# Kernel optimization log

Hardware: AMD Instinct MI355X
Metric: run time of the kernel (lower is better)

The kernel has to match this reference:

```python
import jax, jax.numpy as jnp
import numpy as np

B, N, C, H = 8, 2048, 512, 8
D = C // H                      # head dim = 64
Q_LENGTHS = [1024 + 128 * i for i in range(B)]  # ragged: 1024..1920, sum below
TQ = sum(Q_LENGTHS)             # 11776 total queries


def setup_inputs() -> dict:
    key = jax.random.key(0)
    ks = jax.random.split(key, 5)
    w = 0.02  # init scale for weights
    return {
        "x": jax.random.normal(ks[0], (B, N, C), jnp.float32),
        "q": jax.random.normal(ks[1], (TQ, C), jnp.float32),
        "Wq": jax.random.normal(ks[2], (C, C), jnp.float32) * w,
        "Wkv": jax.random.normal(ks[3], (2 * C, C), jnp.float32) * w,
        "Wproj": jax.random.normal(ks[4], (C, C), jnp.float32) * w,
        "bproj": jnp.zeros((C,), jnp.float32),
        "q_lengths": jnp.array(Q_LENGTHS, jnp.int32),
        "max_q_len": max(Q_LENGTHS),
    }


def reference(x, q, Wq, Wkv, Wproj, bproj, q_lengths, max_q_len):
    # Eval path of Attention.forward: batched_sparse_attention(q, k, v, q_lengths, scale)
    # == varlen cross-attention: queries of batch b attend over all N kv tokens of batch b.
    Tq = q.shape[0]
    scale = D ** -0.5

    qh = (q @ Wq.T).reshape(Tq, H, D)                 # [Tq, H, D]
    kv = (x @ Wkv.T).reshape(B, N, 2, H, D)
    k = kv[:, :, 0]                                   # [B, N, H, D]
    v = kv[:, :, 1]                                   # [B, N, H, D]

    # ragged -> padded per-batch layout
    csum = jnp.cumsum(q_lengths)                      # [B]
    offs = jnp.concatenate([jnp.zeros((1,), csum.dtype), csum])
    tok = jnp.arange(Tq)
    q_batch = (tok[:, None] >= csum[None, :]).sum(-1)  # [Tq] batch id per query
    q_pos = tok - offs[q_batch]                        # [Tq] position within batch

    qpad = jnp.zeros((B, max_q_len, H, D), qh.dtype).at[q_batch, q_pos].set(qh)

    scores = jnp.einsum('blhd,bnhd->bhln', qpad, k) * scale  # [B, H, L, N]
    attn = jax.nn.softmax(scores, axis=-1)                   # all N keys valid
    out = jnp.einsum('bhln,bnhd->blhd', attn, v)             # [B, L, H, D]

    out = out[q_batch, q_pos].reshape(Tq, C)           # gather ragged rows back
    return out @ Wproj.T + bproj
```

## Files before the change

### kernel.cpp

```cpp
#include <hip/hip_runtime.h>
#include <hip/hip_bf16.h>
#include <math.h>

constexpr int Cc = 512;
constexpr int Hh = 8;
constexpr int Dd = 64;
constexpr int Nn = 2048;
constexpr int Bb = 8;
constexpr int GK = 512;

typedef __attribute__((ext_vector_type(8))) short short8;
typedef __attribute__((ext_vector_type(4))) float f32x4;
typedef __attribute__((ext_vector_type(16))) float f32x16;
typedef __attribute__((ext_vector_type(4))) unsigned int u32x4;
typedef __attribute__((ext_vector_type(2))) unsigned int u32x2;

#define C2SCALE 0.1803368801f

static __device__ __forceinline__ ushort f2bf(float v) {
  __hip_bfloat16 h = __float2bfloat16(v);
  return *reinterpret_cast<ushort*>(&h);
}
static __device__ __forceinline__ float bf2f(ushort u) {
  __hip_bfloat16 h = *reinterpret_cast<__hip_bfloat16*>(&u);
  return __bfloat162float(h);
}
static __device__ __forceinline__ unsigned int pk2(float f0, float f1) {
  return (unsigned int)f2bf(f0) | ((unsigned int)f2bf(f1) << 16);
}

template <int MODE, int TERMS, bool AF32, bool BF32>
__global__ __launch_bounds__(256) void mfma_nt2_kernel(
    const void* __restrict__ A0p, const void* __restrict__ A1p,
    const void* __restrict__ B0p, const void* __restrict__ B1p,
    const float* __restrict__ bias, float* __restrict__ Cf,
    ushort* __restrict__ Chi, int Nc)
{
  __shared__ ushort lAh[128 * 32];
  __shared__ ushort lBh[128 * 32];
  __shared__ ushort lAl[TERMS == 3 ? 128 * 32 : 1];
  __shared__ ushort lBl[TERMS == 3 ? 128 * 32 : 1];

  const int tid = threadIdx.x;
  const int w = tid >> 6, lane = tid & 63;
  const int c = lane & 15, g = lane >> 4;
  const int wr = (w >> 1) * 64, wc = (w & 1) * 64;
  const int m0 = blockIdx.y * 128, n0 = blockIdx.x * 128;
  const int sr = tid >> 2;
  const int sk = (tid & 3) * 8;

  short8 rAh[2], rAl[2], rBh[2], rBl[2];

  auto ldf32 = [&](const float* F, size_t idx, short8& h, short8& l) {
    const float4 f0 = *(const float4*)(F + idx);
    const float4 f1 = *(const float4*)(F + idx + 4);
    const float vv[8] = {f0.x, f0.y, f0.z, f0.w, f1.x, f1.y, f1.z, f1.w};
#pragma unroll
    for (int j = 0; j < 8; ++j) {
      const ushort hb = f2bf(vv[j]);
      ((ushort*)&h)[j] = hb;
      if (TERMS == 3) ((ushort*)&l)[j] = f2bf(vv[j] - bf2f(hb));
    }
  };

  auto loadA = [&](int k0) {
#pragma unroll
    for (int hf = 0; hf < 2; ++hf) {
      const size_t idx = (size_t)(m0 + sr + hf * 64) * GK + k0 + sk;
      if (AF32) {
        ldf32((const float*)A0p, idx, rAh[hf], rAl[hf]);
      } else {
        rAh[hf] = *(const short8*)((const ushort*)A0p + idx);
        if (TERMS == 3) rAl[hf] = *(const short8*)((const ushort*)A1p + idx);
      }
    }
  };
  auto loadB = [&](int k0) {
#pragma unroll
    for (int hf = 0; hf < 2; ++hf) {
      const size_t idx = (size_t)(n0 + sr + hf * 64) * GK + k0 + sk;
      if (BF32) {
        ldf32((const float*)B0p, idx, rBh[hf], rBl[hf]);
      } else {
        rBh[hf] = *(const short8*)((const ushort*)B0p + idx);
        if (TERMS == 3) rBl[hf] = *(const short8*)((const ushort*)B1p + idx);
      }
    }
  };

  f32x4 acc[4][4] = {};
  loadA(0);
  loadB(0);

  for (int k0 = 0; k0 < GK; k0 += 32) {
    __syncthreads();
    *(short8*)&lAh[sr * 32 + sk]        = rAh[0];
    *(short8*)&lAh[(sr + 64) * 32 + sk] = rAh[1];
    *(short8*)&lBh[sr * 32 + sk]        = rBh[0];
    *(short8*)&lBh[(sr + 64) * 32 + sk] = rBh[1];
    if (TERMS == 3) {
      *(short8*)&lAl[sr * 32 + sk]        = rAl[0];
      *(short8*)&lAl[(sr + 64) * 32 + sk] = rAl[1];
      *(short8*)&lBl[sr * 32 + sk]        = rBl[0];
      *(short8*)&lBl[(sr + 64) * 32 + sk] = rBl[1];
    }
    __syncthreads();
    if (k0 + 32 < GK) { loadA(k0 + 32); loadB(k0 + 32); }

    short8 ah[4], al[4], bh[4], bl[4];
#pragma unroll
    for (int i = 0; i < 4; ++i) {
      const int ar = (wr + i * 16 + c) * 32 + g * 8;
      const int br = (wc + i * 16 + c) * 32 + g * 8;
      ah[i] = *(const short8*)&lAh[ar];
      bh[i] = *(const short8*)&lBh[br];
      if (TERMS == 3) {
        al[i] = *(const short8*)&lAl[ar];
        bl[i] = *(const short8*)&lBl[br];
      }
    }
#pragma unroll
    for (int mi = 0; mi < 4; ++mi)
#pragma unroll
      for (int nj = 0; nj < 4; ++nj) {
        if (TERMS == 3) {
          acc[mi][nj] = __builtin_amdgcn_mfma_f32_16x16x32_bf16(ah[mi], bl[nj], acc[mi][nj], 0,0,0);
          acc[mi][nj] = __builtin_amdgcn_mfma_f32_16x16x32_bf16(al[mi], bh[nj], acc[mi][nj], 0,0,0);
        }
        acc[mi][nj] = __builtin_amdgcn_mfma_f32_16x16x32_bf16(ah[mi], bh[nj], acc[mi][nj], 0,0,0);
      }
  }

#pragma unroll
  for (int mi = 0; mi < 4; ++mi) {
#pragma unroll
    for (int r = 0; r < 4; ++r) {
      const size_t rb = (size_t)(m0 + wr + mi * 16 + g * 4 + r) * Nc;
#pragma unroll
      for (int nj = 0; nj < 4; ++nj) {
        const int col = n0 + wc + nj * 16 + c;
        const float v = acc[mi][nj][r];
        if (MODE == 0) {
          Cf[rb + col] = v + bias[col];
        } else if (MODE == 1) {
          Chi[rb + col] = f2bf(v);
        } else {
          Chi[rb + col] = f2bf(v * C2SCALE);
        }
      }
    }
  }
}


__global__ __launch_bounds__(256) void attn_mfma8_kernel(
    const ushort* __restrict__ qhi,
    const ushort* __restrict__ kbf,
    const ushort* __restrict__ vtb,
    ushort* __restrict__ ohi,
    ushort* __restrict__ olo)
{
  constexpr int QOFF[8] = {0, 1024, 2176, 3456, 4864, 6400, 8064, 9856};

  const int lin = blockIdx.x;
  const int b  = lin & 7;
  const int h  = (lin >> 3) & 7;
  const int qt = lin >> 6;

  const int Lb  = 1024 + 128 * b;
  const int off = QOFF[b];
  if (qt * 128 >= Lb) return;

  constexpr int KP = 72;
  constexpr int VP = 136;
  constexpr int NC = Nn / 128;
  __shared__ ushort Ks[128 * KP];
  __shared__ ushort Vs[64 * VP];

  const int tid = threadIdx.x;
  const int lane = tid & 63;
  const int w = tid >> 6;
  const int l31 = lane & 31;
  const int hi5 = lane >> 5;

  short8 qfh[4];
  const int qrow = off + qt * 128 + w * 32 + l31;
  {
    const size_t base = (size_t)qrow * Cc + h * Dd + hi5 * 8;
#pragma unroll
    for (int db = 0; db < 4; ++db)
      qfh[db] = *(const short8*)(qhi + base + db * 16);
  }

  float l_s = 0.f;
  f32x16 accO[2] = {};

  const size_t kbase = (size_t)b * Nn * Cc + h * Dd;
  const size_t vbase = (size_t)h * Dd * (Bb * Nn) + (size_t)b * Nn;

  for (int ch = 0; ch < NC; ++ch) {
    __syncthreads();
#pragma unroll
    for (int it = 0; it < 4; ++it) {
      const int i = tid + it * 256;
      const int row = i >> 3, c8 = (i & 7) * 8;
      *(short8*)&Ks[row * KP + c8] =
          *(const short8*)&kbf[kbase + (size_t)(ch * 128 + row) * Cc + c8];
    }
#pragma unroll
    for (int it = 0; it < 4; ++it) {
      const int i = tid + it * 256;
      const int row = i >> 4, c8 = (i & 15) * 8;
      *(short8*)&Vs[row * VP + c8] =
          *(const short8*)&vtb[vbase + (size_t)row * (Bb * Nn) + ch * 128 + c8];
    }
    __syncthreads();

#pragma unroll
    for (int st = 0; st < 2; ++st) {
      f32x16 accT[2] = {};
      __builtin_amdgcn_s_setprio(1);
#pragma unroll
      for (int db = 0; db < 4; ++db) {
#pragma unroll
        for (int kb = 0; kb < 2; ++kb) {
          const short8 kf = *(const short8*)
              &Ks[(st * 64 + kb * 32 + l31) * KP + db * 16 + hi5 * 8];
          accT[kb] = __builtin_amdgcn_mfma_f32_32x32x16_bf16(kf, qfh[db], accT[kb], 0,0,0);
        }
      }
      __builtin_amdgcn_s_setprio(0);

      float ps[4] = {0.f, 0.f, 0.f, 0.f};
#pragma unroll
      for (int kb = 0; kb < 2; ++kb)
#pragma unroll
        for (int r = 0; r < 16; ++r) {
          const float p = __builtin_amdgcn_exp2f(accT[kb][r]);
          accT[kb][r] = p;
          ps[r & 3] += p;
        }
      float psum = (ps[0] + ps[1]) + (ps[2] + ps[3]);
#if __has_builtin(__builtin_amdgcn_permlane32_swap)
      {
        const unsigned int pu = __builtin_bit_cast(unsigned int, psum);
        const u32x2 pr = __builtin_amdgcn_permlane32_swap(pu, pu, false, false);
        psum += __builtin_bit_cast(float, hi5 ? pr[0] : pr[1]);
      }
#else
      psum += __shfl_xor(psum, 32);
#endif
      l_s += psum;

      short8 pa[4];
#pragma unroll
      for (int ks = 0; ks < 4; ++ks) {
        const int kb = ks >> 1, base = (ks & 1) * 8;
        const unsigned int ua = pk2(accT[kb][base + 0], accT[kb][base + 1]);
        const unsigned int uc = pk2(accT[kb][base + 2], accT[kb][base + 3]);
        const unsigned int ub = pk2(accT[kb][base + 4], accT[kb][base + 5]);
        const unsigned int ud = pk2(accT[kb][base + 6], accT[kb][base + 7]);
        u32x4 wv;
#if __has_builtin(__builtin_amdgcn_permlane32_swap)
        const u32x2 r02 = __builtin_amdgcn_permlane32_swap(ua, ub, false, false);
        const u32x2 r13 = __builtin_amdgcn_permlane32_swap(uc, ud, false, false);
        wv.x = r02[0];
        wv.y = r13[0];
        wv.z = r02[1];
        wv.w = r13[1];
#else
        const unsigned int sxa = __shfl_xor(ua, 32);
        const unsigned int sxb = __shfl_xor(ub, 32);
        const unsigned int sxc = __shfl_xor(uc, 32);
        const unsigned int sxd = __shfl_xor(ud, 32);
        wv.x = hi5 ? sxb : ua;
        wv.y = hi5 ? sxd : uc;
        wv.z = hi5 ? ub : sxa;
        wv.w = hi5 ? ud : sxc;
#endif
        pa[ks] = __builtin_bit_cast(short8, wv);
      }

      __builtin_amdgcn_s_setprio(1);
#pragma unroll
      for (int ks = 0; ks < 4; ++ks)
#pragma unroll
        for (int ma = 0; ma < 2; ++ma) {
          const short8 vf = *(const short8*)
              &Vs[(ma * 32 + l31) * VP + st * 64 + ks * 16 + hi5 * 8];
          accO[ma] = __builtin_amdgcn_mfma_f32_32x32x16_bf16(vf, pa[ks], accO[ma], 0,0,0);
        }
      __builtin_amdgcn_s_setprio(0);
    }
  }

  const float inv = 1.f / l_s;
  const size_t rb = (size_t)qrow * Cc + h * Dd;
#pragma unroll
  for (int ma = 0; ma < 2; ++ma) {
#pragma unroll
    for (int g2 = 0; g2 < 4; ++g2) {
      const int d0 = ma * 32 + g2 * 8 + hi5 * 4;
      ushort4 uh, ul;
#pragma unroll
      for (int e = 0; e < 4; ++e) {
        const float o = accO[ma][g2 * 4 + e] * inv;
        const ushort hb = f2bf(o);
        ((ushort*)&uh)[e] = hb;
        ((ushort*)&ul)[e] = f2bf(o - bf2f(hb));
      }
      *(ushort4*)&ohi[rb + d0] = uh;
      *(ushort4*)&olo[rb + d0] = ul;
    }
  }
}

extern "C" void kernel_launch(void* const* d_in, const int* in_sizes, int n_in,
                              void* d_out, int out_size, void* d_ws, size_t ws_size,
                              hipStream_t stream)
{
  const float* x     = (const float*)d_in[0];
  const float* q     = (const float*)d_in[1];
  const float* Wq    = (const float*)d_in[2];
  const float* Wkv   = (const float*)d_in[3];
  const float* Wproj = (const float*)d_in[4];
  const float* bproj = (const float*)d_in[5];

  const int TQ = in_sizes[1] / Cc;
  const int BN = in_sizes[0] / Cc;

  const float* Wv = Wkv + (size_t)Cc * Cc;

  const size_t szQ = (size_t)TQ * Cc * 2;
  const size_t szX = (size_t)BN * Cc * 2;

  char* p = (char*)d_ws;
  ushort* q_hi  = (ushort*)p;  p += szQ;
  ushort* k_bf  = (ushort*)p;  p += szX;
  ushort* v_t   = (ushort*)p;  p += szX;
  ushort* at_hi = (ushort*)p;  p += szQ;
  ushort* at_lo = (ushort*)p;

  mfma_nt2_kernel<2, 1, true, true><<<dim3(Cc/128, TQ/128), 256, 0, stream>>>(
      q, nullptr, Wq, nullptr, nullptr, nullptr, q_hi, Cc);
  mfma_nt2_kernel<1, 1, true, true><<<dim3(Cc/128, BN/128), 256, 0, stream>>>(
      x, nullptr, Wkv, nullptr, nullptr, nullptr, k_bf, Cc);
  mfma_nt2_kernel<1, 1, true, true><<<dim3(BN/128, Cc/128), 256, 0, stream>>>(
      Wv, nullptr, x, nullptr, nullptr, nullptr, v_t, BN);
  attn_mfma8_kernel<<<dim3(64 * 15), 256, 0, stream>>>(
      q_hi, k_bf, v_t, at_hi, at_lo);
  mfma_nt2_kernel<0, 3, false, true><<<dim3(Cc/128, TQ/128), 256, 0, stream>>>(
      at_hi, at_lo, Wproj, nullptr, bproj, (float*)d_out, nullptr, Cc);
}
```

Before: 199.9 us.

## Switch attention to 16x16x32 MFMA with 512-thread blocks and permuted V layout

Rewrites the attention kernel to use 16x16x32 bf16 MFMAs with 8 waves of 16 query rows each, instead of 4 waves of 32 rows using 32x32x16. V is stored into shared memory with a column permutation, so the P accumulator registers can feed the PV MFMA directly without permlane swaps. The row sum is reduced once at the end with shuffles. The intent is to cut the cross-lane shuffle work, lower register pressure and raise occupancy, at the cost of more MFMA instructions and more waves per block.

```diff
diff --git a/kernel.cpp b/kernel.cpp
--- a/kernel.cpp
+++ b/kernel.cpp
@@ -11,7 +11,6 @@
 
 typedef __attribute__((ext_vector_type(8))) short short8;
 typedef __attribute__((ext_vector_type(4))) float f32x4;
-typedef __attribute__((ext_vector_type(16))) float f32x16;
 typedef __attribute__((ext_vector_type(4))) unsigned int u32x4;
 typedef __attribute__((ext_vector_type(2))) unsigned int u32x2;
 
@@ -152,8 +151,7 @@
   }
 }
 
-
-__global__ __launch_bounds__(256) void attn_mfma8_kernel(
+__global__ __launch_bounds__(512, 4) void attn_mfma10_kernel(
     const ushort* __restrict__ qhi,
     const ushort* __restrict__ kbf,
     const ushort* __restrict__ vtb,
@@ -180,20 +178,19 @@
   const int tid = threadIdx.x;
   const int lane = tid & 63;
   const int w = tid >> 6;
-  const int l31 = lane & 31;
-  const int hi5 = lane >> 5;
-
-  short8 qfh[4];
-  const int qrow = off + qt * 128 + w * 32 + l31;
+  const int c = lane & 15;
+  const int g = (lane >> 4) & 3;
+
+  short8 qf[2];
+  const int qrow = off + qt * 128 + w * 16 + c;
   {
-    const size_t base = (size_t)qrow * Cc + h * Dd + hi5 * 8;
-#pragma unroll
-    for (int db = 0; db < 4; ++db)
-      qfh[db] = *(const short8*)(qhi + base + db * 16);
-  }
-
-  float l_s = 0.f;
-  f32x16 accO[2] = {};
+    const size_t base = (size_t)qrow * Cc + h * Dd + g * 8;
+    qf[0] = *(const short8*)(qhi + base);
+    qf[1] = *(const short8*)(qhi + base + 32);
+  }
+
+  float l_part = 0.f;
+  f32x4 accO4[4] = {};
 
   const size_t kbase = (size_t)b * Nn * Cc + h * Dd;
   const size_t vbase = (size_t)h * Dd * (Bb * Nn) + (size_t)b * Nn;
@@ -201,117 +198,93 @@
   for (int ch = 0; ch < NC; ++ch) {
     __syncthreads();
 #pragma unroll
-    for (int it = 0; it < 4; ++it) {
-      const int i = tid + it * 256;
+    for (int it = 0; it < 2; ++it) {
+      const int i = tid + it * 512;
       const int row = i >> 3, c8 = (i & 7) * 8;
       *(short8*)&Ks[row * KP + c8] =
           *(const short8*)&kbf[kbase + (size_t)(ch * 128 + row) * Cc + c8];
     }
 #pragma unroll
-    for (int it = 0; it < 4; ++it) {
-      const int i = tid + it * 256;
+    for (int it = 0; it < 2; ++it) {
+      const int i = tid + it * 512;
       const int row = i >> 4, c8 = (i & 15) * 8;
-      *(short8*)&Vs[row * VP + c8] =
+      const short8 v =
           *(const short8*)&vtb[vbase + (size_t)row * (Bb * Nn) + ch * 128 + c8];
+      const u32x4 vv = __builtin_bit_cast(u32x4, v);
+      u32x2 vlo, vhi;
+      vlo[0] = vv[0]; vlo[1] = vv[1];
+      vhi[0] = vv[2]; vhi[1] = vv[3];
+      const int base = (c8 & ~31) | ((c8 & 8) << 1) | ((c8 & 16) >> 2);
+      *(u32x2*)&Vs[row * VP + base]     = vlo;
+      *(u32x2*)&Vs[row * VP + base + 8] = vhi;
     }
     __syncthreads();
 
 #pragma unroll
     for (int st = 0; st < 2; ++st) {
-      f32x16 accT[2] = {};
+      f32x4 accT4[4] = {};
       __builtin_amdgcn_s_setprio(1);
 #pragma unroll
-      for (int db = 0; db < 4; ++db) {
-#pragma unroll
-        for (int kb = 0; kb < 2; ++kb) {
+      for (int ks2 = 0; ks2 < 2; ++ks2) {
+#pragma unroll
+        for (int kb = 0; kb < 4; ++kb) {
           const short8 kf = *(const short8*)
-              &Ks[(st * 64 + kb * 32 + l31) * KP + db * 16 + hi5 * 8];
-          accT[kb] = __builtin_amdgcn_mfma_f32_32x32x16_bf16(kf, qfh[db], accT[kb], 0,0,0);
+              &Ks[(st * 64 + kb * 16 + c) * KP + ks2 * 32 + g * 8];
+          accT4[kb] = __builtin_amdgcn_mfma_f32_16x16x32_bf16(kf, qf[ks2], accT4[kb], 0,0,0);
         }
       }
       __builtin_amdgcn_s_setprio(0);
 
-      float ps[4] = {0.f, 0.f, 0.f, 0.f};
-#pragma unroll
-      for (int kb = 0; kb < 2; ++kb)
-#pragma unroll
-        for (int r = 0; r < 16; ++r) {
-          const float p = __builtin_amdgcn_exp2f(accT[kb][r]);
-          accT[kb][r] = p;
-          ps[r & 3] += p;
+      unsigned int up[4][2];
+#pragma unroll
+      for (int kb = 0; kb < 4; ++kb) {
+        const float p0 = __builtin_amdgcn_exp2f(accT4[kb][0]);
+        const float p1 = __builtin_amdgcn_exp2f(accT4[kb][1]);
+        const float p2 = __builtin_amdgcn_exp2f(accT4[kb][2]);
+        const float p3 = __builtin_amdgcn_exp2f(accT4[kb][3]);
+        l_part += (p0 + p1) + (p2 + p3);
+        up[kb][0] = pk2(p0, p1);
+        up[kb][1] = pk2(p2, p3);
+      }
+
+#pragma unroll
+      for (int ks2 = 0; ks2 < 2; ++ks2) {
+        u32x4 wv;
+        wv.x = up[2 * ks2][0];
+        wv.y = up[2 * ks2][1];
+        wv.z = up[2 * ks2 + 1][0];
+        wv.w = up[2 * ks2 + 1][1];
+        const short8 pa = __builtin_bit_cast(short8, wv);
+        __builtin_amdgcn_s_setprio(1);
+#pragma unroll
+        for (int db = 0; db < 4; ++db) {
+          const short8 vf = *(const short8*)
+              &Vs[(db * 16 + c) * VP + st * 64 + ks2 * 32 + g * 8];
+          accO4[db] = __builtin_amdgcn_mfma_f32_16x16x32_bf16(vf, pa, accO4[db], 0,0,0);
         }
-      float psum = (ps[0] + ps[1]) + (ps[2] + ps[3]);
-#if __has_builtin(__builtin_amdgcn_permlane32_swap)
-      {
-        const unsigned int pu = __builtin_bit_cast(unsigned int, psum);
-        const u32x2 pr = __builtin_amdgcn_permlane32_swap(pu, pu, false, false);
-        psum += __builtin_bit_cast(float, hi5 ? pr[0] : pr[1]);
-      }
-#else
-      psum += __shfl_xor(psum, 32);
-#endif
-      l_s += psum;
-
-      short8 pa[4];
-#pragma unroll
-      for (int ks = 0; ks < 4; ++ks) {
-        const int kb = ks >> 1, base = (ks & 1) * 8;
-        const unsigned int ua = pk2(accT[kb][base + 0], accT[kb][base + 1]);
-        const unsigned int uc = pk2(accT[kb][base + 2], accT[kb][base + 3]);
-        const unsigned int ub = pk2(accT[kb][base + 4], accT[kb][base + 5]);
-        const unsigned int ud = pk2(accT[kb][base + 6], accT[kb][base + 7]);
-        u32x4 wv;
-#if __has_builtin(__builtin_amdgcn_permlane32_swap)
-        const u32x2 r02 = __builtin_amdgcn_permlane32_swap(ua, ub, false, false);
-        const u32x2 r13 = __builtin_amdgcn_permlane32_swap(uc, ud, false, false);
-        wv.x = r02[0];
-        wv.y = r13[0];
-        wv.z = r02[1];
-        wv.w = r13[1];
-#else
-        const unsigned int sxa = __shfl_xor(ua, 32);
-        const unsigned int sxb = __shfl_xor(ub, 32);
-        const unsigned int sxc = __shfl_xor(uc, 32);
-        const unsigned int sxd = __shfl_xor(ud, 32);
-        wv.x = hi5 ? sxb : ua;
-        wv.y = hi5 ? sxd : uc;
-        wv.z = hi5 ? ub : sxa;
-        wv.w = hi5 ? ud : sxc;
-#endif
-        pa[ks] = __builtin_bit_cast(short8, wv);
-      }
-
-      __builtin_amdgcn_s_setprio(1);
-#pragma unroll
-      for (int ks = 0; ks < 4; ++ks)
-#pragma unroll
-        for (int ma = 0; ma < 2; ++ma) {
-          const short8 vf = *(const short8*)
-              &Vs[(ma * 32 + l31) * VP + st * 64 + ks * 16 + hi5 * 8];
-          accO[ma] = __builtin_amdgcn_mfma_f32_32x32x16_bf16(vf, pa[ks], accO[ma], 0,0,0);
-        }
-      __builtin_amdgcn_s_setprio(0);
-    }
-  }
-
-  const float inv = 1.f / l_s;
+        __builtin_amdgcn_s_setprio(0);
+      }
+    }
+  }
+
+  float l = l_part;
+  l += __shfl_xor(l, 16);
+  l += __shfl_xor(l, 32);
+  const float inv = 1.f / l;
   const size_t rb = (size_t)qrow * Cc + h * Dd;
 #pragma unroll
-  for (int ma = 0; ma < 2; ++ma) {
-#pragma unroll
-    for (int g2 = 0; g2 < 4; ++g2) {
-      const int d0 = ma * 32 + g2 * 8 + hi5 * 4;
-      ushort4 uh, ul;
-#pragma unroll
-      for (int e = 0; e < 4; ++e) {
-        const float o = accO[ma][g2 * 4 + e] * inv;
-        const ushort hb = f2bf(o);
-        ((ushort*)&uh)[e] = hb;
-        ((ushort*)&ul)[e] = f2bf(o - bf2f(hb));
-      }
-      *(ushort4*)&ohi[rb + d0] = uh;
-      *(ushort4*)&olo[rb + d0] = ul;
-    }
+  for (int db = 0; db < 4; ++db) {
+    const int d0 = db * 16 + g * 4;
+    ushort4 uh, ul;
+#pragma unroll
+    for (int e = 0; e < 4; ++e) {
+      const float o = accO4[db][e] * inv;
+      const ushort hb = f2bf(o);
+      ((ushort*)&uh)[e] = hb;
+      ((ushort*)&ul)[e] = f2bf(o - bf2f(hb));
+    }
+    *(ushort4*)&ohi[rb + d0] = uh;
+    *(ushort4*)&olo[rb + d0] = ul;
   }
 }
 
@@ -347,7 +320,7 @@
       x, nullptr, Wkv, nullptr, nullptr, nullptr, k_bf, Cc);
   mfma_nt2_kernel<1, 1, true, true><<<dim3(BN/128, Cc/128), 256, 0, stream>>>(
       Wv, nullptr, x, nullptr, nullptr, nullptr, v_t, BN);
-  attn_mfma8_kernel<<<dim3(64 * 15), 256, 0, stream>>>(
+  attn_mfma10_kernel<<<dim3(64 * 15), 512, 0, stream>>>(
       q_hi, k_bf, v_t, at_hi, at_lo);
   mfma_nt2_kernel<0, 3, false, true><<<dim3(Cc/128, TQ/128), 256, 0, stream>>>(
       at_hi, at_lo, Wproj, nullptr, bproj, (float*)d_out, nullptr, Cc);
```

New measurement: 190.5 us. 1.05x faster.
